# Kernel tuning notes

Measured on AMD Instinct MI355X. Metric: run time of the kernel, lower is better.

## Reference

```python
import jax, jax.numpy as jnp
import numpy as np
from jax import lax

B, T, E = 64, 1024, 512
H, NSTACK = 512, 2


def setup_inputs() -> dict:
    key = jax.random.key(0)
    ks = jax.random.split(key, 7)
    seq = jax.random.normal(ks[0], (B, T, E), dtype=jnp.float32)
    seq_len = jax.random.randint(ks[1], (B,), 1, T + 1)
    seq_len = seq_len.at[0].set(T)  # torch sizes output by max(seq_len); pin it to T
    s = 1.0 / np.sqrt(H)
    W_ih = jax.random.uniform(ks[2], (NSTACK, 4 * H, E), jnp.float32, -s, s)
    W_hh = jax.random.uniform(ks[3], (NSTACK, 4 * H, H), jnp.float32, -s, s)
    b_ih = jax.random.uniform(ks[4], (NSTACK, 4 * H), jnp.float32, -s, s)
    b_hh = jax.random.uniform(ks[5], (NSTACK, 4 * H), jnp.float32, -s, s)
    return {"seq": seq, "seq_len": seq_len, "W_ih": W_ih, "W_hh": W_hh,
            "b_ih": b_ih, "b_hh": b_hh}


def _encoder_step(x, h, c, W_ih, W_hh, b_ih, b_hh):
    """One time step of the nStack residual LSTM. x:[B,E], h/c:[nStack,B,H]."""
    nh, nc = [], []
    inp = x
    for s in range(W_ih.shape[0]):
        gates = inp @ W_ih[s].T + h[s] @ W_hh[s].T + b_ih[s] + b_hh[s]
        i, f, g, o = jnp.split(gates, 4, axis=-1)
        i, f, o = jax.nn.sigmoid(i), jax.nn.sigmoid(f), jax.nn.sigmoid(o)
        g = jnp.tanh(g)
        cs = f * c[s] + i * g
        hs = o * jnp.tanh(cs)
        inp = hs + inp  # residual (E == H)
        nh.append(hs)
        nc.append(cs)
    return inp, jnp.stack(nh), jnp.stack(nc)


def reference(seq, seq_len, W_ih, W_hh, b_ih, b_hh):
    # Masked full-batch recurrence == torch's sorted shrinking-batch loop:
    # inactive rows (t >= seq_len) keep their state and write 0 hiddens.
    b, t, _ = seq.shape
    nstack = W_ih.shape[0]
    hidden = W_hh.shape[-1]
    h0 = jnp.zeros((nstack, b, hidden), seq.dtype)
    c0 = jnp.zeros((nstack, b, hidden), seq.dtype)
    mask_t = jnp.arange(t)[:, None] < seq_len[None, :]  # [T,B]

    def step(carry, xt):
        h, c = carry
        x, m = xt  # x:[B,E], m:[B]
        hx, nh, nc = _encoder_step(x, h, c, W_ih, W_hh, b_ih, b_hh)
        mm = m[None, :, None]
        h = jnp.where(mm, nh, h)
        c = jnp.where(mm, nc, c)
        out = jnp.where(m[:, None], hx, jnp.zeros_like(hx))
        return (h, c), out

    (h, c), outs = lax.scan(step, (h0, c0), (jnp.swapaxes(seq, 0, 1), mask_t))
    total_hiddens = jnp.swapaxes(outs, 0, 1)  # [B,T,H]
    return total_hiddens, h, c
```

## Files before the change

kernel.cpp:

```cpp
#include <hip/hip_runtime.h>
#include <stdint.h>

#define BB 64
#define TT 1024
#define HH 512
typedef unsigned long long ull;
typedef float v4f __attribute__((ext_vector_type(4)));
typedef short v8s __attribute__((ext_vector_type(8)));

__device__ __forceinline__ short f2bf(float f) {
    unsigned u = __float_as_uint(f);
    u += 0x7fffu + ((u >> 16) & 1u);
    return (short)(u >> 16);
}
__device__ __forceinline__ float sigmoidf_(float x) {
    x = fminf(fmaxf(x, -30.f), 30.f);
    return 1.f / (1.f + __expf(-x));
}
__device__ __forceinline__ float tanhf_(float x) {
    x = fminf(fmaxf(x, -15.f), 15.f);
    float e = __expf(2.f * x);
    return (e - 1.f) / (e + 1.f);
}

__device__ __forceinline__ ull aload64(const ull* p) {
    return __hip_atomic_load(p, __ATOMIC_RELAXED, __HIP_MEMORY_SCOPE_AGENT);
}
__device__ __forceinline__ void astore64(ull* p, ull v) {
    __hip_atomic_store(p, v, __ATOMIC_RELAXED, __HIP_MEMORY_SCOPE_AGENT);
}
__device__ __forceinline__ float aloadf(const float* p) {
    return __hip_atomic_load(p, __ATOMIC_RELAXED, __HIP_MEMORY_SCOPE_AGENT);
}
__device__ __forceinline__ void wait_ge(unsigned* c, unsigned tgt) {
    while (__hip_atomic_load(c, __ATOMIC_RELAXED, __HIP_MEMORY_SCOPE_AGENT) < tgt)
        __builtin_amdgcn_s_sleep(1);
}

__global__ __launch_bounds__(512, 2) void lstm_persistent_kernel(
    const float* __restrict__ seq, const int* __restrict__ seq_len,
    const float* __restrict__ W_ih, const float* __restrict__ W_hh,
    const float* __restrict__ b_ih, const float* __restrict__ b_hh,
    float* __restrict__ out, char* __restrict__ ws)
{
    __shared__ __align__(16) short act_lds[2048 * 8];
    __shared__ float gates_lds[4][16][32];
    __shared__ __align__(8) short hstore[16][32];
    __shared__ __align__(8) short istore[16][32];
    __shared__ __align__(8) float fstore[16][32];

    const int gid = blockIdx.x;
    const int g   = gid & 3;
    const int s   = (gid >> 2) & 1;
    const int u0  = (gid >> 3) << 5;
    const int bg  = g << 4;
    const int tid = threadIdx.x;
    const int w   = tid >> 6;
    const int l   = tid & 63;
    const int q   = w >> 1;
    const int uh  = w & 1;
    const int quad = l >> 4, l15 = l & 15;
    const int cb  = tid >> 5, cu = tid & 31;

    unsigned* cnt0 = (unsigned*)ws + g * 64;
    unsigned* cnt1 = cnt0 + 32;
    short* h0b = (short*)(ws + 1024);
    short* h1b = h0b + 4 * 4 * 16 * 512;
    short* ib  = h1b + 4 * 4 * 16 * 512;
    float* ifb = (float*)(ib + 4 * 4 * 16 * 512);

    const float* Wi = W_ih + (size_t)s * (2048 * 512);
    const float* Wh = W_hh + (size_t)s * (2048 * 512);
    const int row = q * 512 + u0 + uh * 16 + l15;
    v8s wf[32];
#pragma unroll
    for (int kt = 0; kt < 32; ++kt) {
        int ko = kt * 32 + quad * 8;
        const float* p = (ko < 512) ? (Wi + (size_t)row * 512 + ko)
                                    : (Wh + (size_t)row * 512 + (ko - 512));
        float4 x0 = *(const float4*)p;
        float4 x1 = *(const float4*)(p + 4);
        v8s v;
        v[0]=f2bf(x0.x); v[1]=f2bf(x0.y); v[2]=f2bf(x0.z); v[3]=f2bf(x0.w);
        v[4]=f2bf(x1.x); v[5]=f2bf(x1.y); v[6]=f2bf(x1.z); v[7]=f2bf(x1.w);
        wf[kt] = v;
    }
    float bias[4];
#pragma unroll
    for (int qq = 0; qq < 4; ++qq)
        bias[qq] = b_ih[s * 2048 + qq * 512 + u0 + cu] + b_hh[s * 2048 + qq * 512 + u0 + cu];
    const int len = seq_len[bg + cb];
    float hreg = 0.f, creg = 0.f;
    short* myhb = (s == 0) ? h0b : h1b;

    for (int tau = 0; tau <= TT; ++tau) {
        if (s == 0 && tau >= TT) break;
        if (s == 1 && tau == 0) continue;
        const int t   = (s == 0) ? tau : tau - 1;
        const int rsl = (tau - 1) & 3;
        const int wsl = tau & 3;
        float xres = 0.f;

        if (s == 0) {
#pragma unroll
            for (int j = 0; j < 2; ++j) {
                int c = (j << 9) + tid;
                int ll = c & 63, m = ll & 15;
                int ko = ((c >> 6) << 5) + ((ll >> 4) << 3);
                const float* p = seq + (((size_t)(bg + m) * TT + t) << 9) + ko;
                float4 x0 = *(const float4*)p, x1 = *(const float4*)(p + 4);
                v8s v;
                v[0]=f2bf(x0.x); v[1]=f2bf(x0.y); v[2]=f2bf(x0.z); v[3]=f2bf(x0.w);
                v[4]=f2bf(x1.x); v[5]=f2bf(x1.y); v[6]=f2bf(x1.z); v[7]=f2bf(x1.w);
                *(v8s*)(act_lds + (size_t)c * 8) = v;
            }
            xres = seq[(((size_t)(bg + cb) * TT + t) << 9) + u0 + cu];
            if (tid == 0) {
                if (tau >= 1) wait_ge(cnt0, 16u * tau);
                if (tau >= 3) wait_ge(cnt1, 16u * (tau - 2));
            }
        } else {
            if (tid == 0) {
                wait_ge(cnt0, 16u * tau);
                if (tau >= 2) wait_ge(cnt1, 16u * (tau - 1));
            }
        }
        __syncthreads();

        if (s == 1) {
#pragma unroll
            for (int j = 0; j < 2; ++j) {
                int c = (j << 9) + tid;
                int ll = c & 63, m = ll & 15;
                int ko = ((c >> 6) << 5) + ((ll >> 4) << 3);
                const ull* p = (const ull*)(ib + (((((rsl << 2) | g) << 4) + m) << 9) + ko);
                ull a = aload64(p), b = aload64(p + 1);
                *(ull*)(act_lds + (size_t)c * 8) = a;
                *((ull*)(act_lds + (size_t)c * 8) + 1) = b;
            }
        }
        if (tau == (s == 0 ? 0 : 1)) {
#pragma unroll
            for (int j = 2; j < 4; ++j) {
                int c = (j << 9) + tid;
                *(ull*)(act_lds + (size_t)c * 8) = 0ull;
                *((ull*)(act_lds + (size_t)c * 8) + 1) = 0ull;
            }
        } else {
#pragma unroll
            for (int j = 2; j < 4; ++j) {
                int c = (j << 9) + tid;
                int ll = c & 63, m = ll & 15;
                int ko = ((c >> 6) << 5) + ((ll >> 4) << 3) - 512;
                const ull* p = (const ull*)(myhb + (((((rsl << 2) | g) << 4) + m) << 9) + ko);
                ull a = aload64(p), b = aload64(p + 1);
                *(ull*)(act_lds + (size_t)c * 8) = a;
                *((ull*)(act_lds + (size_t)c * 8) + 1) = b;
            }
        }
        __syncthreads();

        v4f z = {0.f, 0.f, 0.f, 0.f};
        v4f acc0 = z, acc1 = z, acc2 = z, acc3 = z;
#pragma unroll
        for (int kt = 0; kt < 32; kt += 4) {
            v8s a0 = *(const v8s*)(act_lds + ((kt + 0) * 64 + l) * 8);
            v8s a1 = *(const v8s*)(act_lds + ((kt + 1) * 64 + l) * 8);
            v8s a2 = *(const v8s*)(act_lds + ((kt + 2) * 64 + l) * 8);
            v8s a3 = *(const v8s*)(act_lds + ((kt + 3) * 64 + l) * 8);
            acc0 = __builtin_amdgcn_mfma_f32_16x16x32_bf16(a0, wf[kt + 0], acc0, 0, 0, 0);
            acc1 = __builtin_amdgcn_mfma_f32_16x16x32_bf16(a1, wf[kt + 1], acc1, 0, 0, 0);
            acc2 = __builtin_amdgcn_mfma_f32_16x16x32_bf16(a2, wf[kt + 2], acc2, 0, 0, 0);
            acc3 = __builtin_amdgcn_mfma_f32_16x16x32_bf16(a3, wf[kt + 3], acc3, 0, 0, 0);
        }
        v4f af = (acc0 + acc1) + (acc2 + acc3);
#pragma unroll
        for (int r = 0; r < 4; ++r)
            gates_lds[q][quad * 4 + r][uh * 16 + l15] = af[r];
        __syncthreads();

        float gi = gates_lds[0][cb][cu] + bias[0];
        float gf = gates_lds[1][cb][cu] + bias[1];
        float gg = gates_lds[2][cb][cu] + bias[2];
        float go = gates_lds[3][cb][cu] + bias[3];
        float ii = sigmoidf_(gi), ff = sigmoidf_(gf);
        float gv = tanhf_(gg),   oo = sigmoidf_(go);
        float cs = ff * creg + ii * gv;
        float hs = oo * tanhf_(cs);
        const bool msk = (t < len);
        if (msk) { creg = cs; hreg = hs; }
        if (s == 0) {
            float i1 = hs + xres;
            hstore[cb][cu] = f2bf(hreg);
            istore[cb][cu] = f2bf(i1);
            fstore[cb][cu] = i1;
        } else {
            float i1 = aloadf(ifb + (((((rsl << 2) | g) << 4) + cb) << 9) + u0 + cu);
            out[(((size_t)(bg + cb) * TT + t) << 9) + u0 + cu] = msk ? (i1 + hs) : 0.f;
            hstore[cb][cu] = f2bf(hreg);
        }
        __syncthreads();

        const int base = (((wsl << 2) | g) << 4);
        if (s == 0) {
            if (tid < 128) {
                int r = tid >> 3, o = (tid & 7) << 2;
                astore64((ull*)(h0b + ((base + r) << 9) + u0 + o), *(const ull*)&hstore[r][o]);
            } else if (tid < 256) {
                int t2 = tid - 128; int r = t2 >> 3, o = (t2 & 7) << 2;
                astore64((ull*)(ib + ((base + r) << 9) + u0 + o), *(const ull*)&istore[r][o]);
            } else {
                int t2 = tid - 256; int r = t2 >> 4, o = (t2 & 15) << 1;
                astore64((ull*)(ifb + ((base + r) << 9) + u0 + o), *(const ull*)&fstore[r][o]);
            }
        } else {
            if (tid < 128) {
                int r = tid >> 3, o = (tid & 7) << 2;
                astore64((ull*)(h1b + ((base + r) << 9) + u0 + o), *(const ull*)&hstore[r][o]);
            }
        }
        asm volatile("s_waitcnt vmcnt(0)" ::: "memory");
        __syncthreads();
        if (tid == 0)
            __hip_atomic_fetch_add((s == 0) ? cnt0 : cnt1, 1u,
                                   __ATOMIC_RELAXED, __HIP_MEMORY_SCOPE_AGENT);
    }

    const size_t OH = (size_t)BB * TT * HH;
    const size_t hoff = OH + (size_t)s * BB * HH + ((size_t)(bg + cb) << 9) + u0 + cu;
    out[hoff] = hreg;
    out[hoff + (size_t)2 * BB * HH] = creg;
}

extern "C" void kernel_launch(void* const* d_in, const int* in_sizes, int n_in,
                              void* d_out, int out_size, void* d_ws, size_t ws_size,
                              hipStream_t stream) {
    const float* seq     = (const float*)d_in[0];
    const int*   seq_len = (const int*)d_in[1];
    const float* W_ih    = (const float*)d_in[2];
    const float* W_hh    = (const float*)d_in[3];
    const float* b_ih    = (const float*)d_in[4];
    const float* b_hh    = (const float*)d_in[5];
    float* out = (float*)d_out;

    hipMemsetAsync(d_ws, 0, 1024, stream);

    lstm_persistent_kernel<<<dim3(128), dim3(512), 0, stream>>>(
        seq, seq_len, W_ih, W_hh, b_ih, b_hh, out, (char*)d_ws);
}
```

Baseline: 4.869 ms.

## Replace counter barriers with per-element tagged data flags for LSTM handoff

```diff
diff --git a/kernel.cpp b/kernel.cpp
--- a/kernel.cpp
+++ b/kernel.cpp
@@ -7,6 +7,7 @@
 typedef unsigned long long ull;
 typedef float v4f __attribute__((ext_vector_type(4)));
 typedef short v8s __attribute__((ext_vector_type(8)));
+typedef unsigned v4u __attribute__((ext_vector_type(4)));
 
 __device__ __forceinline__ short f2bf(float f) {
     unsigned u = __float_as_uint(f);
@@ -23,21 +24,56 @@
     return (e - 1.f) / (e + 1.f);
 }
 
-__device__ __forceinline__ ull aload64(const ull* p) {
-    return __hip_atomic_load(p, __ATOMIC_RELAXED, __HIP_MEMORY_SCOPE_AGENT);
-}
-__device__ __forceinline__ void astore64(ull* p, ull v) {
-    __hip_atomic_store(p, v, __ATOMIC_RELAXED, __HIP_MEMORY_SCOPE_AGENT);
-}
-__device__ __forceinline__ float aloadf(const float* p) {
+__device__ __forceinline__ unsigned aload32(const unsigned* p) {
     return __hip_atomic_load(p, __ATOMIC_RELAXED, __HIP_MEMORY_SCOPE_AGENT);
 }
 __device__ __forceinline__ void wait_ge(unsigned* c, unsigned tgt) {
     while (__hip_atomic_load(c, __ATOMIC_RELAXED, __HIP_MEMORY_SCOPE_AGENT) < tgt)
         __builtin_amdgcn_s_sleep(1);
 }
-
-__global__ __launch_bounds__(512, 2) void lstm_persistent_kernel(
+__device__ __forceinline__ void stcc(unsigned* p, unsigned v) {
+    asm volatile("global_store_dword %0, %1, off sc0 sc1" :: "v"(p), "v"(v) : "memory");
+}
+__device__ __forceinline__ void ld4cc(const unsigned* p, v4u& r0, v4u& r1, v4u& r2, v4u& r3) {
+    asm volatile(
+        "global_load_dwordx4 %0, %4, off sc0 sc1\n\t"
+        "global_load_dwordx4 %1, %4, off offset:16 sc0 sc1\n\t"
+        "global_load_dwordx4 %2, %4, off offset:2048 sc0 sc1\n\t"
+        "global_load_dwordx4 %3, %4, off offset:2064 sc0 sc1\n\t"
+        "s_waitcnt vmcnt(0)"
+        : "=&v"(r0), "=&v"(r1), "=&v"(r2), "=&v"(r3)
+        : "v"(p) : "memory");
+}
+__device__ __forceinline__ void ld8cc(const unsigned* px, const unsigned* ph,
+        v4u& x0, v4u& x1, v4u& x2, v4u& x3, v4u& h0, v4u& h1, v4u& h2, v4u& h3) {
+    asm volatile(
+        "global_load_dwordx4 %0, %8, off sc0 sc1\n\t"
+        "global_load_dwordx4 %1, %8, off offset:16 sc0 sc1\n\t"
+        "global_load_dwordx4 %2, %8, off offset:2048 sc0 sc1\n\t"
+        "global_load_dwordx4 %3, %8, off offset:2064 sc0 sc1\n\t"
+        "global_load_dwordx4 %4, %9, off sc0 sc1\n\t"
+        "global_load_dwordx4 %5, %9, off offset:16 sc0 sc1\n\t"
+        "global_load_dwordx4 %6, %9, off offset:2048 sc0 sc1\n\t"
+        "global_load_dwordx4 %7, %9, off offset:2064 sc0 sc1\n\t"
+        "s_waitcnt vmcnt(0)"
+        : "=&v"(x0), "=&v"(x1), "=&v"(x2), "=&v"(x3),
+          "=&v"(h0), "=&v"(h1), "=&v"(h2), "=&v"(h3)
+        : "v"(px), "v"(ph) : "memory");
+}
+__device__ __forceinline__ unsigned tagdiff(v4u a, v4u b, unsigned tg) {
+    return ((a.x ^ tg) | (a.y ^ tg) | (a.z ^ tg) | (a.w ^ tg) |
+            (b.x ^ tg) | (b.y ^ tg) | (b.z ^ tg) | (b.w ^ tg)) & 0xFFFFu;
+}
+__device__ __forceinline__ void packlds(short* dst, v4u a, v4u b) {
+    v4u d;
+    d.x = (a.x >> 16) | (a.y & 0xFFFF0000u);
+    d.y = (a.z >> 16) | (a.w & 0xFFFF0000u);
+    d.z = (b.x >> 16) | (b.y & 0xFFFF0000u);
+    d.w = (b.z >> 16) | (b.w & 0xFFFF0000u);
+    *(v4u*)dst = d;
+}
+
+__global__ __launch_bounds__(512, 1) void lstm_persistent_kernel(
     const float* __restrict__ seq, const int* __restrict__ seq_len,
     const float* __restrict__ W_ih, const float* __restrict__ W_hh,
     const float* __restrict__ b_ih, const float* __restrict__ b_hh,
@@ -45,9 +81,6 @@
 {
     __shared__ __align__(16) short act_lds[2048 * 8];
     __shared__ float gates_lds[4][16][32];
-    __shared__ __align__(8) short hstore[16][32];
-    __shared__ __align__(8) short istore[16][32];
-    __shared__ __align__(8) float fstore[16][32];
 
     const int gid = blockIdx.x;
     const int g   = gid & 3;
@@ -62,12 +95,10 @@
     const int quad = l >> 4, l15 = l & 15;
     const int cb  = tid >> 5, cu = tid & 31;
 
-    unsigned* cnt0 = (unsigned*)ws + g * 64;
-    unsigned* cnt1 = cnt0 + 32;
-    short* h0b = (short*)(ws + 1024);
-    short* h1b = h0b + 4 * 4 * 16 * 512;
-    short* ib  = h1b + 4 * 4 * 16 * 512;
-    float* ifb = (float*)(ib + 4 * 4 * 16 * 512);
+    unsigned* rc1 = (unsigned*)(ws + g * 256);
+    unsigned* h0b = (unsigned*)(ws + 1024);
+    unsigned* h1b = h0b + 4 * 4 * 16 * 512;
+    unsigned* ibb = h1b + 4 * 4 * 16 * 512;
 
     const float* Wi = W_ih + (size_t)s * (2048 * 512);
     const float* Wh = W_hh + (size_t)s * (2048 * 512);
@@ -91,17 +122,27 @@
         bias[qq] = b_ih[s * 2048 + qq * 512 + u0 + cu] + b_hh[s * 2048 + qq * 512 + u0 + cu];
     const int len = seq_len[bg + cb];
     float hreg = 0.f, creg = 0.f;
-    short* myhb = (s == 0) ? h0b : h1b;
+
+    const int ch0 = 1024 + (tid << 1);
+    const int mh  = ch0 & 15;
+    const int kh  = (((ch0 >> 6) << 5) + (((ch0 >> 4) & 3) << 3)) - 512;
+    const int cx0 = tid << 1;
+    const int mx  = cx0 & 15;
+    const int kx  = ((cx0 >> 6) << 5) + (((cx0 >> 4) & 3) << 3);
+    unsigned* myhb = (s == 0) ? h0b : h1b;
 
     for (int tau = 0; tau <= TT; ++tau) {
         if (s == 0 && tau >= TT) break;
         if (s == 1 && tau == 0) continue;
         const int t   = (s == 0) ? tau : tau - 1;
-        const int rsl = (tau - 1) & 3;
-        const int wsl = tau & 3;
+        const int rb  = (((tau - 1) & 3) << 2 | g) << 13;
+        const int wb  = ((tau & 3) << 2 | g) << 13;
+        const unsigned tg = (unsigned)(tau - 1);
         float xres = 0.f;
+        unsigned rcv = 0xFFFFFFFFu;
 
         if (s == 0) {
+            if (tid == 0 && tau >= 4) rcv = aload32(rc1);
 #pragma unroll
             for (int j = 0; j < 2; ++j) {
                 int c = (j << 9) + tid;
@@ -115,50 +156,56 @@
                 *(v8s*)(act_lds + (size_t)c * 8) = v;
             }
             xres = seq[(((size_t)(bg + cb) * TT + t) << 9) + u0 + cu];
-            if (tid == 0) {
-                if (tau >= 1) wait_ge(cnt0, 16u * tau);
-                if (tau >= 3) wait_ge(cnt1, 16u * (tau - 2));
+            if (tau == 0) {
+                v4u zz = {0, 0, 0, 0};
+                *(v4u*)(act_lds + (size_t)ch0 * 8) = zz;
+                *(v4u*)(act_lds + (size_t)(ch0 + 1) * 8) = zz;
+            } else {
+                const unsigned* hp = h0b + rb + (mh << 9) + kh;
+                for (;;) {
+                    v4u r0, r1, r2, r3;
+                    ld4cc(hp, r0, r1, r2, r3);
+                    if ((tagdiff(r0, r1, tg) | tagdiff(r2, r3, tg)) == 0) {
+                        packlds(act_lds + (size_t)ch0 * 8, r0, r1);
+                        packlds(act_lds + (size_t)(ch0 + 1) * 8, r2, r3);
+                        break;
+                    }
+                }
             }
         } else {
-            if (tid == 0) {
-                wait_ge(cnt0, 16u * tau);
-                if (tau >= 2) wait_ge(cnt1, 16u * (tau - 1));
+            const unsigned* px = ibb + rb + (mx << 9) + kx;
+            if (tau == 1) {
+                v4u zz = {0, 0, 0, 0};
+                *(v4u*)(act_lds + (size_t)ch0 * 8) = zz;
+                *(v4u*)(act_lds + (size_t)(ch0 + 1) * 8) = zz;
+                for (;;) {
+                    v4u r0, r1, r2, r3;
+                    ld4cc(px, r0, r1, r2, r3);
+                    if ((tagdiff(r0, r1, tg) | tagdiff(r2, r3, tg)) == 0) {
+                        packlds(act_lds + (size_t)cx0 * 8, r0, r1);
+                        packlds(act_lds + (size_t)(cx0 + 1) * 8, r2, r3);
+                        break;
+                    }
+                }
+            } else {
+                const unsigned* ph = h1b + rb + (mh << 9) + kh;
+                for (;;) {
+                    v4u x0, x1, x2, x3, h0, h1, h2, h3;
+                    ld8cc(px, ph, x0, x1, x2, x3, h0, h1, h2, h3);
+                    if ((tagdiff(x0, x1, tg) | tagdiff(x2, x3, tg) |
+                         tagdiff(h0, h1, tg) | tagdiff(h2, h3, tg)) == 0) {
+                        packlds(act_lds + (size_t)cx0 * 8, x0, x1);
+                        packlds(act_lds + (size_t)(cx0 + 1) * 8, x2, x3);
+                        packlds(act_lds + (size_t)ch0 * 8, h0, h1);
+                        packlds(act_lds + (size_t)(ch0 + 1) * 8, h2, h3);
+                        break;
+                    }
+                }
             }
         }
         __syncthreads();
-
-        if (s == 1) {
-#pragma unroll
-            for (int j = 0; j < 2; ++j) {
-                int c = (j << 9) + tid;
-                int ll = c & 63, m = ll & 15;
-                int ko = ((c >> 6) << 5) + ((ll >> 4) << 3);
-                const ull* p = (const ull*)(ib + (((((rsl << 2) | g) << 4) + m) << 9) + ko);
-                ull a = aload64(p), b = aload64(p + 1);
-                *(ull*)(act_lds + (size_t)c * 8) = a;
-                *((ull*)(act_lds + (size_t)c * 8) + 1) = b;
-            }
-        }
-        if (tau == (s == 0 ? 0 : 1)) {
-#pragma unroll
-            for (int j = 2; j < 4; ++j) {
-                int c = (j << 9) + tid;
-                *(ull*)(act_lds + (size_t)c * 8) = 0ull;
-                *((ull*)(act_lds + (size_t)c * 8) + 1) = 0ull;
-            }
-        } else {
-#pragma unroll
-            for (int j = 2; j < 4; ++j) {
-                int c = (j << 9) + tid;
-                int ll = c & 63, m = ll & 15;
-                int ko = ((c >> 6) << 5) + ((ll >> 4) << 3) - 512;
-                const ull* p = (const ull*)(myhb + (((((rsl << 2) | g) << 4) + m) << 9) + ko);
-                ull a = aload64(p), b = aload64(p + 1);
-                *(ull*)(act_lds + (size_t)c * 8) = a;
-                *((ull*)(act_lds + (size_t)c * 8) + 1) = b;
-            }
-        }
-        __syncthreads();
+        if (s == 1 && tid == 0)
+            __hip_atomic_fetch_add(rc1, 1u, __ATOMIC_RELAXED, __HIP_MEMORY_SCOPE_AGENT);
 
         v4f z = {0.f, 0.f, 0.f, 0.f};
         v4f acc0 = z, acc1 = z, acc2 = z, acc3 = z;
@@ -189,41 +236,30 @@
         float hs = oo * tanhf_(cs);
         const bool msk = (t < len);
         if (msk) { creg = cs; hreg = hs; }
+        float i1s = 0.f;
         if (s == 0) {
-            float i1 = hs + xres;
-            hstore[cb][cu] = f2bf(hreg);
-            istore[cb][cu] = f2bf(i1);
-            fstore[cb][cu] = i1;
+            i1s = hs + xres;
         } else {
-            float i1 = aloadf(ifb + (((((rsl << 2) | g) << 4) + cb) << 9) + u0 + cu);
+            int k  = u0 + cu;
+            int cI = ((k >> 5) << 6) + (((k >> 3) & 3) << 4) + cb;
+            unsigned short us = (unsigned short)act_lds[cI * 8 + (k & 7)];
+            float i1 = __uint_as_float(((unsigned)us) << 16);
             out[(((size_t)(bg + cb) * TT + t) << 9) + u0 + cu] = msk ? (i1 + hs) : 0.f;
-            hstore[cb][cu] = f2bf(hreg);
+        }
+        if (s == 0 && tid == 0 && tau >= 4) {
+            unsigned need = 16u * (unsigned)(tau - 3);
+            if (rcv < need) wait_ge(rc1, need);
         }
         __syncthreads();
 
-        const int base = (((wsl << 2) | g) << 4);
+        const unsigned otg = (unsigned)tau;
+        const int widx = wb + (cb << 9) + u0 + cu;
         if (s == 0) {
-            if (tid < 128) {
-                int r = tid >> 3, o = (tid & 7) << 2;
-                astore64((ull*)(h0b + ((base + r) << 9) + u0 + o), *(const ull*)&hstore[r][o]);
-            } else if (tid < 256) {
-                int t2 = tid - 128; int r = t2 >> 3, o = (t2 & 7) << 2;
-                astore64((ull*)(ib + ((base + r) << 9) + u0 + o), *(const ull*)&istore[r][o]);
-            } else {
-                int t2 = tid - 256; int r = t2 >> 4, o = (t2 & 15) << 1;
-                astore64((ull*)(ifb + ((base + r) << 9) + u0 + o), *(const ull*)&fstore[r][o]);
-            }
+            stcc(h0b + widx, (((unsigned)(unsigned short)f2bf(hreg)) << 16) | otg);
+            stcc(ibb + widx, (((unsigned)(unsigned short)f2bf(i1s)) << 16) | otg);
         } else {
-            if (tid < 128) {
-                int r = tid >> 3, o = (tid & 7) << 2;
-                astore64((ull*)(h1b + ((base + r) << 9) + u0 + o), *(const ull*)&hstore[r][o]);
-            }
-        }
-        asm volatile("s_waitcnt vmcnt(0)" ::: "memory");
-        __syncthreads();
-        if (tid == 0)
-            __hip_atomic_fetch_add((s == 0) ? cnt0 : cnt1, 1u,
-                                   __ATOMIC_RELAXED, __HIP_MEMORY_SCOPE_AGENT);
+            stcc(h1b + widx, (((unsigned)(unsigned short)f2bf(hreg)) << 16) | otg);
+        }
     }
 
     const size_t OH = (size_t)BB * TT * HH;
```

New measurement: 4.090 ms. -16.0%, faster.
